# Kernel optimization log

Measured on AMD Instinct MI355X. Metric: run time of the kernel, lower is better.

## Reference

```python
import jax, jax.numpy as jnp
import numpy as np

# Scalar quantization params (QLinear __init__ args)
FEATURE_BITWIDTH = 8
WEIGHT_BITWIDTH = 8
INPUT_ZERO_POINT = -3
OUTPUT_ZERO_POINT = -5
INPUT_SCALE = 0.05
OUTPUT_SCALE = 0.1
QMIN = -(1 << (FEATURE_BITWIDTH - 1))   # -128
QMAX = (1 << (FEATURE_BITWIDTH - 1)) - 1  # 127

M, K, N = 8192, 4096, 4096


def float_to_fixed_point(x, bitwidth):
    """Represent x (0 < x < 1) as int_scale * 2^-frac_bits with int_scale
    in [2^(bitwidth-2), 2^(bitwidth-1)) (mantissa fits in signed `bitwidth` bits)."""
    frac_bits = (bitwidth - 1 - jnp.ceil(jnp.log2(x))).astype(jnp.int32)
    int_scale = jnp.round(x * jnp.exp2(frac_bits.astype(jnp.float32))).astype(jnp.int32)
    return int_scale, frac_bits


def setup_inputs() -> dict:
    key = jax.random.key(0)
    k1, k2, k3, k4 = jax.random.split(key, 4)
    qinput = jax.random.randint(k1, (M, K), -128, 128, dtype=jnp.int8)
    qweight = jax.random.randint(k2, (N, K), -128, 128, dtype=jnp.int8)
    qbias = jax.random.randint(k3, (N,), -(1 << 16), 1 << 16, dtype=jnp.int32)
    # per-output-channel weight scale; keeps folded scale in (0, 1)
    weight_scale = jax.random.uniform(k4, (N,), jnp.float32, 0.002, 0.02)
    return {"qinput": qinput, "qweight": qweight, "qbias": qbias,
            "weight_scale": weight_scale}


def reference(qinput, qweight, qbias, weight_scale):
    w32 = qweight.astype(jnp.int32)                      # [N, K]
    # Qbias' = qbias - sum_k(qweight) * Zin  (bias shift folding input zero point)
    shifted_qbias = qbias - w32.sum(axis=1) * INPUT_ZERO_POINT  # [N]
    # int32 GEMM: [M, K] @ [K, N] + bias
    acc = qinput.astype(jnp.int32) @ w32.T + shifted_qbias[None, :]  # [M, N]
    # fixed-point requantization: (acc * int_scale) >> frac_bits + Zout
    folded_scale = INPUT_SCALE * weight_scale / OUTPUT_SCALE         # [N], in (0,1)
    int_scale, frac_bits = float_to_fixed_point(folded_scale, FEATURE_BITWIDTH)
    # widen to int64 for the multiply so the (acc * int_scale) product cannot wrap
    prod = acc.astype(jnp.int64) * int_scale.astype(jnp.int64)[None, :]
    scaled = jnp.right_shift(prod, frac_bits.astype(jnp.int64)[None, :])  # arithmetic >>
    out = scaled + OUTPUT_ZERO_POINT
    return jnp.clip(out, QMIN, QMAX).astype(jnp.int8)
```

## Files before the change

### kernel.cpp

```cpp
#include <hip/hip_runtime.h>
#include <cstdint>
#include <cstddef>

#define M_DIM 8192
#define N_DIM 4096
#define K_DIM 4096

#define BM 128
#define BN 128
#define BK 128

#define BM2 256
#define BN2 256
#define BK2 128
#define NKT (K_DIM / BK2)

typedef int int32x4 __attribute__((ext_vector_type(4)));


typedef __attribute__((address_space(1))) const void* gas_cptr;
typedef __attribute__((address_space(3))) void* las_ptr;

__device__ __forceinline__ void async_copy16(const void* g, void* l) {
    __builtin_amdgcn_global_load_lds((gas_cptr)g, (las_ptr)l, 16, 0, 0);
}

__device__ __forceinline__ int32x4 pack16(const int* p) {
    const int32x4* v = (const int32x4*)p;
    int32x4 w0 = v[0], w1 = v[1], w2 = v[2], w3 = v[3];
    int32x4 r;
    r.x = (w0.x & 0xFF) | ((w0.y & 0xFF) << 8) | ((w0.z & 0xFF) << 16) | (w0.w << 24);
    r.y = (w1.x & 0xFF) | ((w1.y & 0xFF) << 8) | ((w1.z & 0xFF) << 16) | (w1.w << 24);
    r.z = (w2.x & 0xFF) | ((w2.y & 0xFF) << 8) | ((w2.z & 0xFF) << 16) | (w2.w << 24);
    r.w = (w3.x & 0xFF) | ((w3.y & 0xFF) << 8) | ((w3.z & 0xFF) << 16) | (w3.w << 24);
    return r;
}

__global__ void ql_detect_kernel(const int* a, const int* b, int* ws) {
    int t = threadIdx.x;
    int fa = 0, fb = 0;
    for (int i = t; i < 4096; i += 64) {
        int va = a[i]; if (va > 127 || va < -128) fa = 1;
        int vb = b[i]; if (vb > 127 || vb < -128) fb = 1;
    }
    unsigned long long ba = __ballot(fa);
    unsigned long long bb = __ballot(fb);
    if (t == 0) { ws[0] = ba ? 1 : 0; ws[1] = bb ? 1 : 0; }
}

__global__ __launch_bounds__(256)
void ql_pack_kernel(const void* src, int* dst, const int* ws, int flag_idx, long ndw) {
    const int f8 = __builtin_amdgcn_readfirstlane(ws[flag_idx]);
    if (f8) return;
    const long stride = (long)gridDim.x * 256;
    for (long c = (long)blockIdx.x * 256 + threadIdx.x; c < ndw; c += stride) {
        int32x4 v = ((const int32x4*)src)[c];
        dst[c] = (v.x & 0xFF) | ((v.y & 0xFF) << 8) | ((v.z & 0xFF) << 16) | (v.w << 24);
    }
}

__global__ void ql_prep8_kernel(const void* worig, const int8_t* w8p, const int* qbias,
                                const float* wscale, int* ws) {
    const int fb = __builtin_amdgcn_readfirstlane(ws[1]);
    const int8_t* w8 = fb ? (const int8_t*)worig : w8p;

    const int lane = threadIdx.x & 63;
    const int wid  = threadIdx.x >> 6;
    const int n = blockIdx.x * 4 + wid;

    const int32x4* row = (const int32x4*)(w8 + (size_t)n * K_DIM);
    int s = 0;
    for (int c = lane; c < K_DIM / 16; c += 64) {
        int32x4 v = row[c];
#pragma unroll
        for (int j = 0; j < 4; ++j) {
            int w = (j == 0) ? v.x : (j == 1) ? v.y : (j == 2) ? v.z : v.w;
            s += (int)(int8_t)(w) + (int)(int8_t)(w >> 8)
               + (int)(int8_t)(w >> 16) + (w >> 24);
        }
    }
#pragma unroll
    for (int off = 32; off > 0; off >>= 1) s += __shfl_down(s, off, 64);

    if (lane == 0) {
        ws[16 + n] = qbias[n] + 3 * s;
        float folded = (0.05f * wscale[n]) / 0.1f;
        int fbits = (int)(7.0f - ceilf(log2f(folded)));
        int isc = (int)rintf(folded * exp2f((float)fbits));
        ws[16 + N_DIM + n] = isc;
        ws[16 + 2 * N_DIM + n] = fbits;
    }
}

__global__ void ql_prep_kernel(const void* wptr, const int* qbias,
                               const float* wscale, int* ws) {
    const int lane = threadIdx.x & 63;
    const int wid  = threadIdx.x >> 6;
    const int n = blockIdx.x * 4 + wid;
    const int b8 = __builtin_amdgcn_readfirstlane(ws[1]);

    int s = 0;
    if (b8) {
        const int32x4* row = (const int32x4*)((const int8_t*)wptr + (size_t)n * K_DIM);
        for (int c = lane; c < K_DIM / 16; c += 64) {
            int32x4 v = row[c];
#pragma unroll
            for (int j = 0; j < 4; ++j) {
                int w = (j == 0) ? v.x : (j == 1) ? v.y : (j == 2) ? v.z : v.w;
                s += (int)(int8_t)(w) + (int)(int8_t)(w >> 8)
                   + (int)(int8_t)(w >> 16) + (w >> 24);
            }
        }
    } else {
        const int32x4* row = (const int32x4*)((const int*)wptr + (size_t)n * K_DIM);
        for (int c = lane; c < K_DIM / 4; c += 64) {
            int32x4 v = row[c];
            s += v.x + v.y + v.z + v.w;
        }
    }
#pragma unroll
    for (int off = 32; off > 0; off >>= 1) s += __shfl_down(s, off, 64);

    if (lane == 0) {
        ws[16 + n] = qbias[n] + 3 * s;
        float folded = (0.05f * wscale[n]) / 0.1f;
        int fbits = (int)(7.0f - ceilf(log2f(folded)));
        int isc = (int)rintf(folded * exp2f((float)fbits));
        ws[16 + N_DIM + n] = isc;
        ws[16 + 2 * N_DIM + n] = fbits;
    }
}

__device__ __forceinline__ void ql_epilogue(int32x4 acc[4][4], const int* ws,
                                            int* out, int bm, int bn,
                                            int wm, int wn, int qm, int qh) {
    const int* qb  = ws + 16;
    const int* isc = ws + 16 + N_DIM;
    const int* fbt = ws + 16 + 2 * N_DIM;
#pragma unroll
    for (int j = 0; j < 4; ++j) {
        const int n_g = bn * BN + wn + j * 16 + qm;
        const int b0 = qb[n_g];
        const int s0 = isc[n_g];
        const int f0 = fbt[n_g];
#pragma unroll
        for (int i = 0; i < 4; ++i) {
            const int m_base = bm * BM + wm + i * 16 + qh * 4;
#pragma unroll
            for (int r = 0; r < 4; ++r) {
                int v = ((r == 0) ? acc[i][j].x : (r == 1) ? acc[i][j].y
                        : (r == 2) ? acc[i][j].z : acc[i][j].w) + b0;
                long long p = (long long)v * (long long)s0;
                int o = (int)(p >> f0) - 5;
                o = o < -128 ? -128 : (o > 127 ? 127 : o);
                out[(size_t)(m_base + r) * N_DIM + n_g] = o;
            }
        }
    }
}

__device__ __forceinline__ void stage_half8(const int8_t* src, int row0, int tt,
                                            int h, int32x4* Lbuf, int t) {
    const int k0 = tt * BK2;
#pragma unroll
    for (int r = 0; r < 2; ++r) {
        const int c    = h * 1024 + r * 512 + t;
        const int row  = c >> 3;
        const int colg = (c & 7) ^ (row & 7);
        const size_t off = (size_t)(row0 + row) * K_DIM + k0 + colg * 16;
        async_copy16(src + off, &Lbuf[c]);
    }
}

__global__ __launch_bounds__(512, 2)
void ql_gemm8_kernel(const void* a0, const int8_t* a8,
                     const void* b0, const int8_t* w8,
                     const int* ws, int* out) {
    __shared__ int32x4 LA[2][2048];
    __shared__ int32x4 LB[2][2048];

    const int fa = __builtin_amdgcn_readfirstlane(ws[0]);
    const int fb = __builtin_amdgcn_readfirstlane(ws[1]);
    const int8_t* aptr = fa ? (const int8_t*)a0 : a8;
    const int8_t* bptr = fb ? (const int8_t*)b0 : w8;

    const int t    = threadIdx.x;
    const int lane = t & 63;
    const int wid  = t >> 6;
    const int wr   = wid >> 2;
    const int wc   = wid & 3;
    const int qm   = lane & 15;
    const int qh   = lane >> 4;

    const int bn = blockIdx.x;
    const int bm = blockIdx.y;
    const int arow0 = bm * BM2;
    const int brow0 = bn * BN2;

    int32x4 acc[8][4] = {};
    int32x4 af0[4][2], af1[4][2], bf0[2][2], bf1[2][2];

    stage_half8(aptr, arow0, 0, 0, &LA[0][0], t);
    stage_half8(bptr, brow0, 0, 0, &LB[0][0], t);
    stage_half8(aptr, arow0, 0, 1, &LA[0][0], t);
    stage_half8(bptr, brow0, 0, 1, &LB[0][0], t);
    stage_half8(aptr, arow0, 1, 0, &LA[1][0], t);
    stage_half8(bptr, brow0, 1, 0, &LB[1][0], t);

    for (int T = 0; T < NKT; ++T) {
        const int cur = T & 1;
        if (T < NKT - 1) asm volatile("s_waitcnt vmcnt(4)");
        else             asm volatile("s_waitcnt vmcnt(0)");
        __builtin_amdgcn_s_barrier();

#pragma unroll
        for (int i = 0; i < 4; ++i) {
            const int ra = wr * 128 + i * 16 + qm;
#pragma unroll
            for (int s = 0; s < 2; ++s)
                af0[i][s] = LA[cur][ra * 8 + ((s * 4 + qh) ^ (ra & 7))];
        }
#pragma unroll
        for (int j = 0; j < 2; ++j) {
            const int rb = wc * 64 + j * 16 + qm;
#pragma unroll
            for (int s = 0; s < 2; ++s)
                bf0[j][s] = LB[cur][rb * 8 + ((s * 4 + qh) ^ (rb & 7))];
        }
        if (T + 1 < NKT) stage_half8(aptr, arow0, T + 1, 1, &LA[cur ^ 1][0], t);
        __builtin_amdgcn_s_barrier();
        __builtin_amdgcn_s_setprio(1);
#pragma unroll
        for (int s = 0; s < 2; ++s)
#pragma unroll
            for (int i = 0; i < 4; ++i)
#pragma unroll
                for (int j = 0; j < 2; ++j)
                    acc[i][j] = __builtin_amdgcn_mfma_i32_16x16x64_i8(
                        af0[i][s], bf0[j][s], acc[i][j], 0, 0, 0);
        __builtin_amdgcn_s_setprio(0);
        __builtin_amdgcn_s_barrier();

#pragma unroll
        for (int j = 0; j < 2; ++j) {
            const int rb = wc * 64 + (j + 2) * 16 + qm;
#pragma unroll
            for (int s = 0; s < 2; ++s)
                bf1[j][s] = LB[cur][rb * 8 + ((s * 4 + qh) ^ (rb & 7))];
        }
        if (T + 1 < NKT) stage_half8(bptr, brow0, T + 1, 1, &LB[cur ^ 1][0], t);
        __builtin_amdgcn_s_barrier();
        __builtin_amdgcn_s_setprio(1);
#pragma unroll
        for (int s = 0; s < 2; ++s)
#pragma unroll
            for (int i = 0; i < 4; ++i)
#pragma unroll
                for (int j = 0; j < 2; ++j)
                    acc[i][j + 2] = __builtin_amdgcn_mfma_i32_16x16x64_i8(
                        af0[i][s], bf1[j][s], acc[i][j + 2], 0, 0, 0);
        __builtin_amdgcn_s_setprio(0);
        __builtin_amdgcn_s_barrier();

#pragma unroll
        for (int i = 0; i < 4; ++i) {
            const int ra = wr * 128 + (i + 4) * 16 + qm;
#pragma unroll
            for (int s = 0; s < 2; ++s)
                af1[i][s] = LA[cur][ra * 8 + ((s * 4 + qh) ^ (ra & 7))];
        }
        if (T + 2 < NKT) stage_half8(aptr, arow0, T + 2, 0, &LA[cur][0], t);
        __builtin_amdgcn_s_barrier();
        __builtin_amdgcn_s_setprio(1);
#pragma unroll
        for (int s = 0; s < 2; ++s)
#pragma unroll
            for (int i = 0; i < 4; ++i)
#pragma unroll
                for (int j = 0; j < 2; ++j)
                    acc[i + 4][j] = __builtin_amdgcn_mfma_i32_16x16x64_i8(
                        af1[i][s], bf0[j][s], acc[i + 4][j], 0, 0, 0);
        __builtin_amdgcn_s_setprio(0);
        __builtin_amdgcn_s_barrier();

        if (T + 2 < NKT) stage_half8(bptr, brow0, T + 2, 0, &LB[cur][0], t);
        __builtin_amdgcn_s_barrier();
        __builtin_amdgcn_s_setprio(1);
#pragma unroll
        for (int s = 0; s < 2; ++s)
#pragma unroll
            for (int i = 0; i < 4; ++i)
#pragma unroll
                for (int j = 0; j < 2; ++j)
                    acc[i + 4][j + 2] = __builtin_amdgcn_mfma_i32_16x16x64_i8(
                        af1[i][s], bf1[j][s], acc[i + 4][j + 2], 0, 0, 0);
        __builtin_amdgcn_s_setprio(0);
    }

    const int* qb  = ws + 16;
    const int* isc = ws + 16 + N_DIM;
    const int* fbt = ws + 16 + 2 * N_DIM;
#pragma unroll
    for (int j = 0; j < 4; ++j) {
        const int n_g = bn * BN2 + wc * 64 + j * 16 + qm;
        const int b0r = qb[n_g];
        const int s0r = isc[n_g];
        const int f0r = fbt[n_g];
#pragma unroll
        for (int i = 0; i < 8; ++i) {
            const int m_base = bm * BM2 + wr * 128 + i * 16 + qh * 4;
#pragma unroll
            for (int r = 0; r < 4; ++r) {
                int v = ((r == 0) ? acc[i][j].x : (r == 1) ? acc[i][j].y
                        : (r == 2) ? acc[i][j].z : acc[i][j].w) + b0r;
                long long p = (long long)v * (long long)s0r;
                int o = (int)(p >> f0r) - 5;
                o = o < -128 ? -128 : (o > 127 ? 127 : o);
                out[(size_t)(m_base + r) * N_DIM + n_g] = o;
            }
        }
    }
}

__global__ __launch_bounds__(256)
void ql_gemm_fb_kernel(const void* aptr, const void* bptr, const int* ws, int* out) {
    __shared__ int32x4 Als[BM * BK / 16];
    __shared__ int32x4 Bls[BN * BK / 16];

    const int a8 = __builtin_amdgcn_readfirstlane(ws[0]);
    const int b8 = __builtin_amdgcn_readfirstlane(ws[1]);

    const int t    = threadIdx.x;
    const int lane = t & 63;
    const int wid  = t >> 6;
    const int bn = blockIdx.x;
    const int bm = blockIdx.y;

    const int wm = (wid >> 1) * 64;
    const int wn = (wid & 1) * 64;
    const int qm = lane & 15;
    const int qh = lane >> 4;

    int32x4 acc[4][4] = {};

    for (int kt = 0; kt < K_DIM / BK; ++kt) {
        __syncthreads();
        const int k0 = kt * BK;
#pragma unroll
        for (int r = 0; r < 4; ++r) {
            const int c    = r * 256 + t;
            const int row  = c >> 3;
            const int colg = (c & 7) ^ (row & 7);
            const size_t offA = (size_t)(bm * BM + row) * K_DIM + k0 + colg * 16;
            const size_t offB = (size_t)(bn * BN + row) * K_DIM + k0 + colg * 16;
            if (a8) async_copy16((const int8_t*)aptr + offA, &Als[c]);
            else    Als[c] = pack16((const int*)aptr + offA);
            if (b8) async_copy16((const int8_t*)bptr + offB, &Bls[c]);
            else    Bls[c] = pack16((const int*)bptr + offB);
        }
        __syncthreads();

#pragma unroll
        for (int s = 0; s < 2; ++s) {
            const int colk = s * 4 + qh;
            int32x4 af[4], bf[4];
#pragma unroll
            for (int i = 0; i < 4; ++i) {
                const int ra = wm + i * 16 + qm;
                const int rb = wn + i * 16 + qm;
                af[i] = Als[ra * 8 + (colk ^ (ra & 7))];
                bf[i] = Bls[rb * 8 + (colk ^ (rb & 7))];
            }
#pragma unroll
            for (int i = 0; i < 4; ++i)
#pragma unroll
                for (int j = 0; j < 4; ++j)
                    acc[i][j] = __builtin_amdgcn_mfma_i32_16x16x64_i8(
                        af[i], bf[j], acc[i][j], 0, 0, 0);
        }
    }
    ql_epilogue(acc, ws, out, bm, bn, wm, wn, qm, qh);
}

extern "C" void kernel_launch(void* const* d_in, const int* in_sizes, int n_in,
                              void* d_out, int out_size, void* d_ws, size_t ws_size,
                              hipStream_t stream) {
    const void* qin    = d_in[0];
    const void* qwt    = d_in[1];
    const int* qbias   = (const int*)d_in[2];
    const float* wscal = (const float*)d_in[3];
    int* ws  = (int*)d_ws;
    int* out = (int*)d_out;

    hipLaunchKernelGGL(ql_detect_kernel, dim3(1), dim3(64), 0, stream,
                       (const int*)qin, (const int*)qwt, ws);

    const size_t need = 65536 + (size_t)M_DIM * K_DIM + (size_t)N_DIM * K_DIM;
    if (ws_size >= need) {
        int8_t* a8 = (int8_t*)d_ws + 65536;
        int8_t* w8 = a8 + (size_t)M_DIM * K_DIM;
        const long ndwA = (long)M_DIM * K_DIM / 4;
        const long ndwW = (long)N_DIM * K_DIM / 4;
        hipLaunchKernelGGL(ql_pack_kernel, dim3((unsigned)(ndwW / (256 * 4))), dim3(256),
                           0, stream, qwt, (int*)w8, ws, 1, ndwW);
        hipLaunchKernelGGL(ql_pack_kernel, dim3((unsigned)(ndwA / (256 * 4))), dim3(256),
                           0, stream, qin, (int*)a8, ws, 0, ndwA);
        hipLaunchKernelGGL(ql_prep8_kernel, dim3(N_DIM / 4), dim3(256), 0, stream,
                           qwt, w8, qbias, wscal, ws);
        hipLaunchKernelGGL(ql_gemm8_kernel, dim3(N_DIM / BN2, M_DIM / BM2), dim3(512),
                           0, stream, qin, a8, qwt, w8, ws, out);
    } else {
        hipLaunchKernelGGL(ql_prep_kernel, dim3(N_DIM / 4), dim3(256), 0, stream,
                           qwt, qbias, wscal, ws);
        hipLaunchKernelGGL(ql_gemm_fb_kernel, dim3(N_DIM / BN, M_DIM / BM), dim3(256), 0, stream,
                           qin, qwt, ws, out);
    }
}
```

Before: 410.6 us.

## Switch GEMM to 32x32x32 int8 MFMA with precomputed LDS offsets and merge pack kernels

Replaces the 16x16x64 int8 MFMA tiling with 32x32x32 MFMA: each wave keeps a 4x2 array of 16-wide accumulators and loads fragments through precomputed swizzled LDS offsets. Global staging addresses are hoisted into per-thread base pointers, and the K loop is unrolled by two with a peeled tail so the waitcnt counts are constant. The two int32-to-int8 pack launches are merged into one kernel. Fewer, larger MFMAs should cut LDS fragment traffic and issue overhead per FLOP, at the cost of more accumulator registers and a changed epilogue index mapping.

```diff
diff --git a/kernel.cpp b/kernel.cpp
--- a/kernel.cpp
+++ b/kernel.cpp
@@ -15,7 +15,8 @@
 #define BK2 128
 #define NKT (K_DIM / BK2)
 
-typedef int int32x4 __attribute__((ext_vector_type(4)));
+typedef int int32x4  __attribute__((ext_vector_type(4)));
+typedef int int32x16 __attribute__((ext_vector_type(16)));
 
 
 typedef __attribute__((address_space(1))) const void* gas_cptr;
@@ -49,13 +50,23 @@
 }
 
 __global__ __launch_bounds__(256)
-void ql_pack_kernel(const void* src, int* dst, const int* ws, int flag_idx, long ndw) {
-    const int f8 = __builtin_amdgcn_readfirstlane(ws[flag_idx]);
-    if (f8) return;
+void ql_pack2_kernel(const void* wsrc, int* wdst, const void* asrc, int* adst,
+                     const int* ws, long ndwW, long ndwA) {
+    const int fA = __builtin_amdgcn_readfirstlane(ws[0]);
+    const int fW = __builtin_amdgcn_readfirstlane(ws[1]);
+    const long nW = fW ? 0 : ndwW;
+    const long nA = fA ? 0 : ndwA;
+    const long total = nW + nA;
     const long stride = (long)gridDim.x * 256;
-    for (long c = (long)blockIdx.x * 256 + threadIdx.x; c < ndw; c += stride) {
-        int32x4 v = ((const int32x4*)src)[c];
-        dst[c] = (v.x & 0xFF) | ((v.y & 0xFF) << 8) | ((v.z & 0xFF) << 16) | (v.w << 24);
+    for (long c = (long)blockIdx.x * 256 + threadIdx.x; c < total; c += stride) {
+        if (c < nW) {
+            int32x4 v = ((const int32x4*)wsrc)[c];
+            wdst[c] = (v.x & 0xFF) | ((v.y & 0xFF) << 8) | ((v.z & 0xFF) << 16) | (v.w << 24);
+        } else {
+            const long ca = c - nW;
+            int32x4 v = ((const int32x4*)asrc)[ca];
+            adst[ca] = (v.x & 0xFF) | ((v.y & 0xFF) << 8) | ((v.z & 0xFF) << 16) | (v.w << 24);
+        }
     }
 }
 
@@ -159,18 +170,60 @@
     }
 }
 
-__device__ __forceinline__ void stage_half8(const int8_t* src, int row0, int tt,
-                                            int h, int32x4* Lbuf, int t) {
-    const int k0 = tt * BK2;
-#pragma unroll
-    for (int r = 0; r < 2; ++r) {
-        const int c    = h * 1024 + r * 512 + t;
-        const int row  = c >> 3;
-        const int colg = (c & 7) ^ (row & 7);
-        const size_t off = (size_t)(row0 + row) * K_DIM + k0 + colg * 16;
-        async_copy16(src + off, &Lbuf[c]);
-    }
-}
+
+#define LOAD_AF(BUF, MH) do { \
+    _Pragma("unroll") for (int ml = 0; ml < 2; ++ml) \
+    _Pragma("unroll") for (int kc = 0; kc < 4; ++kc) \
+        af[ml][kc] = LA[BUF][baseAe[kc] + (MH) * 512 + ml * 256]; \
+} while (0)
+
+#define LOAD_BF(BUF, NH, DST) do { \
+    _Pragma("unroll") for (int kc = 0; kc < 4; ++kc) \
+        DST[kc] = LB[BUF][baseBe[kc] + (NH) * 256]; \
+} while (0)
+
+#define MFMA_QUAD(MH, NH, BF) do { \
+    __builtin_amdgcn_s_setprio(1); \
+    _Pragma("unroll") for (int kc = 0; kc < 4; ++kc) \
+    _Pragma("unroll") for (int ml = 0; ml < 2; ++ml) \
+        acc[(MH) * 2 + ml][NH] = __builtin_amdgcn_mfma_i32_32x32x32_i8( \
+            af[ml][kc], BF[kc], acc[(MH) * 2 + ml][NH], 0, 0, 0); \
+    __builtin_amdgcn_s_setprio(0); \
+} while (0)
+
+#define STAGE_A(BUF, H, TT) do { \
+    async_copy16(gA + (size_t)(TT) * 128 + (H) * 524288,          &LA[BUF][(H) * 1024 + t]); \
+    async_copy16(gA + (size_t)(TT) * 128 + (H) * 524288 + 262144, &LA[BUF][(H) * 1024 + 512 + t]); \
+} while (0)
+
+#define STAGE_B(BUF, H, TT) do { \
+    async_copy16(gB + (size_t)(TT) * 128 + (H) * 524288,          &LB[BUF][(H) * 1024 + t]); \
+    async_copy16(gB + (size_t)(TT) * 128 + (H) * 524288 + 262144, &LB[BUF][(H) * 1024 + 512 + t]); \
+} while (0)
+
+#define TILE_BODY(BUF, TT, VMC) do { \
+    asm volatile("s_waitcnt vmcnt(" #VMC ")"); \
+    __builtin_amdgcn_s_barrier(); \
+    LOAD_AF(BUF, 0); \
+    LOAD_BF(BUF, 0, bf0); \
+    if ((TT) + 1 < NKT) { STAGE_A(BUF ^ 1, 1, (TT) + 1); } \
+    __builtin_amdgcn_s_barrier(); \
+    MFMA_QUAD(0, 0, bf0); \
+    __builtin_amdgcn_s_barrier(); \
+    LOAD_BF(BUF, 1, bf1); \
+    if ((TT) + 1 < NKT) { STAGE_B(BUF ^ 1, 1, (TT) + 1); } \
+    __builtin_amdgcn_s_barrier(); \
+    MFMA_QUAD(0, 1, bf1); \
+    __builtin_amdgcn_s_barrier(); \
+    LOAD_AF(BUF, 1); \
+    if ((TT) + 2 < NKT) { STAGE_B(BUF, 0, (TT) + 2); } \
+    __builtin_amdgcn_s_barrier(); \
+    MFMA_QUAD(1, 0, bf0); \
+    __builtin_amdgcn_s_barrier(); \
+    if ((TT) + 2 < NKT) { STAGE_A(BUF, 0, (TT) + 2); } \
+    __builtin_amdgcn_s_barrier(); \
+    MFMA_QUAD(1, 1, bf1); \
+} while (0)
 
 __global__ __launch_bounds__(512, 2)
 void ql_gemm8_kernel(const void* a0, const int8_t* a8,
@@ -189,134 +242,63 @@
     const int wid  = t >> 6;
     const int wr   = wid >> 2;
     const int wc   = wid & 3;
-    const int qm   = lane & 15;
-    const int qh   = lane >> 4;
+    const int l31  = lane & 31;
+    const int hi   = lane >> 5;
 
     const int bn = blockIdx.x;
     const int bm = blockIdx.y;
     const int arow0 = bm * BM2;
     const int brow0 = bn * BN2;
 
-    int32x4 acc[8][4] = {};
-    int32x4 af0[4][2], af1[4][2], bf0[2][2], bf1[2][2];
-
-    stage_half8(aptr, arow0, 0, 0, &LA[0][0], t);
-    stage_half8(bptr, brow0, 0, 0, &LB[0][0], t);
-    stage_half8(aptr, arow0, 0, 1, &LA[0][0], t);
-    stage_half8(bptr, brow0, 0, 1, &LB[0][0], t);
-    stage_half8(aptr, arow0, 1, 0, &LA[1][0], t);
-    stage_half8(bptr, brow0, 1, 0, &LB[1][0], t);
-
-    for (int T = 0; T < NKT; ++T) {
-        const int cur = T & 1;
-        if (T < NKT - 1) asm volatile("s_waitcnt vmcnt(4)");
-        else             asm volatile("s_waitcnt vmcnt(0)");
-        __builtin_amdgcn_s_barrier();
-
-#pragma unroll
-        for (int i = 0; i < 4; ++i) {
-            const int ra = wr * 128 + i * 16 + qm;
-#pragma unroll
-            for (int s = 0; s < 2; ++s)
-                af0[i][s] = LA[cur][ra * 8 + ((s * 4 + qh) ^ (ra & 7))];
-        }
-#pragma unroll
-        for (int j = 0; j < 2; ++j) {
-            const int rb = wc * 64 + j * 16 + qm;
-#pragma unroll
-            for (int s = 0; s < 2; ++s)
-                bf0[j][s] = LB[cur][rb * 8 + ((s * 4 + qh) ^ (rb & 7))];
-        }
-        if (T + 1 < NKT) stage_half8(aptr, arow0, T + 1, 1, &LA[cur ^ 1][0], t);
-        __builtin_amdgcn_s_barrier();
-        __builtin_amdgcn_s_setprio(1);
-#pragma unroll
-        for (int s = 0; s < 2; ++s)
-#pragma unroll
-            for (int i = 0; i < 4; ++i)
-#pragma unroll
-                for (int j = 0; j < 2; ++j)
-                    acc[i][j] = __builtin_amdgcn_mfma_i32_16x16x64_i8(
-                        af0[i][s], bf0[j][s], acc[i][j], 0, 0, 0);
-        __builtin_amdgcn_s_setprio(0);
-        __builtin_amdgcn_s_barrier();
-
-#pragma unroll
-        for (int j = 0; j < 2; ++j) {
-            const int rb = wc * 64 + (j + 2) * 16 + qm;
-#pragma unroll
-            for (int s = 0; s < 2; ++s)
-                bf1[j][s] = LB[cur][rb * 8 + ((s * 4 + qh) ^ (rb & 7))];
-        }
-        if (T + 1 < NKT) stage_half8(bptr, brow0, T + 1, 1, &LB[cur ^ 1][0], t);
-        __builtin_amdgcn_s_barrier();
-        __builtin_amdgcn_s_setprio(1);
-#pragma unroll
-        for (int s = 0; s < 2; ++s)
-#pragma unroll
-            for (int i = 0; i < 4; ++i)
-#pragma unroll
-                for (int j = 0; j < 2; ++j)
-                    acc[i][j + 2] = __builtin_amdgcn_mfma_i32_16x16x64_i8(
-                        af0[i][s], bf1[j][s], acc[i][j + 2], 0, 0, 0);
-        __builtin_amdgcn_s_setprio(0);
-        __builtin_amdgcn_s_barrier();
-
-#pragma unroll
-        for (int i = 0; i < 4; ++i) {
-            const int ra = wr * 128 + (i + 4) * 16 + qm;
-#pragma unroll
-            for (int s = 0; s < 2; ++s)
-                af1[i][s] = LA[cur][ra * 8 + ((s * 4 + qh) ^ (ra & 7))];
-        }
-        if (T + 2 < NKT) stage_half8(aptr, arow0, T + 2, 0, &LA[cur][0], t);
-        __builtin_amdgcn_s_barrier();
-        __builtin_amdgcn_s_setprio(1);
-#pragma unroll
-        for (int s = 0; s < 2; ++s)
-#pragma unroll
-            for (int i = 0; i < 4; ++i)
-#pragma unroll
-                for (int j = 0; j < 2; ++j)
-                    acc[i + 4][j] = __builtin_amdgcn_mfma_i32_16x16x64_i8(
-                        af1[i][s], bf0[j][s], acc[i + 4][j], 0, 0, 0);
-        __builtin_amdgcn_s_setprio(0);
-        __builtin_amdgcn_s_barrier();
-
-        if (T + 2 < NKT) stage_half8(bptr, brow0, T + 2, 0, &LB[cur][0], t);
-        __builtin_amdgcn_s_barrier();
-        __builtin_amdgcn_s_setprio(1);
-#pragma unroll
-        for (int s = 0; s < 2; ++s)
-#pragma unroll
-            for (int i = 0; i < 4; ++i)
-#pragma unroll
-                for (int j = 0; j < 2; ++j)
-                    acc[i + 4][j + 2] = __builtin_amdgcn_mfma_i32_16x16x64_i8(
-                        af1[i][s], bf1[j][s], acc[i + 4][j + 2], 0, 0, 0);
-        __builtin_amdgcn_s_setprio(0);
-    }
+    int baseAe[4], baseBe[4];
+#pragma unroll
+    for (int kc = 0; kc < 4; ++kc) {
+        const int phys = (kc * 2 + hi) ^ (lane & 7);
+        baseAe[kc] = (wr * 128 + l31) * 8 + phys;
+        baseBe[kc] = (wc * 64  + l31) * 8 + phys;
+    }
+
+    const int colg = (t & 7) ^ ((t >> 3) & 7);
+    const int8_t* gA = aptr + (size_t)(arow0 + (t >> 3)) * K_DIM + colg * 16;
+    const int8_t* gB = bptr + (size_t)(brow0 + (t >> 3)) * K_DIM + colg * 16;
+
+    int32x16 acc[4][2] = {};
+    int32x4 af[2][4], bf0[4], bf1[4];
+
+    STAGE_A(0, 0, 0); STAGE_B(0, 0, 0);
+    STAGE_A(0, 1, 0); STAGE_B(0, 1, 0);
+    STAGE_A(1, 0, 1); STAGE_B(1, 0, 1);
+
+#pragma unroll 1
+    for (int T = 0; T < NKT - 4; T += 2) {
+        TILE_BODY(0, T, 4);
+        TILE_BODY(1, T + 1, 4);
+    }
+    TILE_BODY(0, NKT - 4, 4);
+    TILE_BODY(1, NKT - 3, 4);
+    TILE_BODY(0, NKT - 2, 4);
+    TILE_BODY(1, NKT - 1, 0);
 
     const int* qb  = ws + 16;
     const int* isc = ws + 16 + N_DIM;
     const int* fbt = ws + 16 + 2 * N_DIM;
 #pragma unroll
-    for (int j = 0; j < 4; ++j) {
-        const int n_g = bn * BN2 + wc * 64 + j * 16 + qm;
+    for (int j = 0; j < 2; ++j) {
+        const int n_g = bn * BN2 + wc * 64 + j * 32 + l31;
         const int b0r = qb[n_g];
         const int s0r = isc[n_g];
         const int f0r = fbt[n_g];
 #pragma unroll
-        for (int i = 0; i < 8; ++i) {
-            const int m_base = bm * BM2 + wr * 128 + i * 16 + qh * 4;
-#pragma unroll
-            for (int r = 0; r < 4; ++r) {
-                int v = ((r == 0) ? acc[i][j].x : (r == 1) ? acc[i][j].y
-                        : (r == 2) ? acc[i][j].z : acc[i][j].w) + b0r;
+        for (int i = 0; i < 4; ++i) {
+            const int m0 = bm * BM2 + wr * 128 + i * 32 + hi * 4;
+#pragma unroll
+            for (int reg = 0; reg < 16; ++reg) {
+                const int row = (reg & 3) + 8 * (reg >> 2);
+                int v = acc[i][j][reg] + b0r;
                 long long p = (long long)v * (long long)s0r;
                 int o = (int)(p >> f0r) - 5;
                 o = o < -128 ? -128 : (o > 127 ? 127 : o);
-                out[(size_t)(m_base + r) * N_DIM + n_g] = o;
+                out[(size_t)(m0 + row) * N_DIM + n_g] = o;
             }
         }
     }
@@ -401,10 +383,9 @@
         int8_t* w8 = a8 + (size_t)M_DIM * K_DIM;
         const long ndwA = (long)M_DIM * K_DIM / 4;
         const long ndwW = (long)N_DIM * K_DIM / 4;
-        hipLaunchKernelGGL(ql_pack_kernel, dim3((unsigned)(ndwW / (256 * 4))), dim3(256),
-                           0, stream, qwt, (int*)w8, ws, 1, ndwW);
-        hipLaunchKernelGGL(ql_pack_kernel, dim3((unsigned)(ndwA / (256 * 4))), dim3(256),
-                           0, stream, qin, (int*)a8, ws, 0, ndwA);
+        const long ndwT = ndwA + ndwW;
+        hipLaunchKernelGGL(ql_pack2_kernel, dim3((unsigned)(ndwT / (256 * 4))), dim3(256),
+                           0, stream, qwt, (int*)w8, qin, (int*)a8, ws, ndwW, ndwA);
         hipLaunchKernelGGL(ql_prep8_kernel, dim3(N_DIM / 4), dim3(256), 0, stream,
                            qwt, w8, qbias, wscal, ws);
         hipLaunchKernelGGL(ql_gemm8_kernel, dim3(N_DIM / BN2, M_DIM / BM2), dim3(512),
```

Result: slower. 426.1 us (+3.8%).
